# Optimization experiments

Measured on AMD Instinct MI355X. Metric: run time of the kernel, lower is better.

Reference implementation:

```python
import jax, jax.numpy as jnp
import numpy as np

NEG_INF = -10000.0
ALPHA = 0.2      # LeakyReLU slope
EPS = 1e-5       # LayerNorm eps
B, N, D = 8, 2048, 128


def setup_inputs() -> dict:
    key = jax.random.key(0)
    ks = jax.random.split(key, 8)
    x = jax.random.normal(ks[0], (B, N, D), dtype=jnp.float32)
    adj_bool = jax.random.randint(ks[1], (B, N, N), 0, 2, dtype=jnp.int32)
    node_mask = jax.random.randint(ks[2], (B, N), 0, 2, dtype=jnp.int32)
    s = 1.0 / np.sqrt(D)
    W = jax.random.uniform(ks[3], (D, D), jnp.float32, -s, s)    # fc weight (in->out)
    a_l = jax.random.uniform(ks[4], (D,), jnp.float32, -s, s)    # attn_l weight
    a_r = jax.random.uniform(ks[5], (D,), jnp.float32, -s, s)    # attn_r weight
    gamma = jnp.ones((D,), jnp.float32)                          # LayerNorm weight
    beta = jnp.zeros((D,), jnp.float32)                          # LayerNorm bias
    return {"x": x, "adj_bool": adj_bool, "node_mask": node_mask,
            "W": W, "a_l": a_l, "a_r": a_r, "gamma": gamma, "beta": beta}


def reference(x, adj_bool, node_mask, W, a_l, a_r, gamma, beta):
    m = node_mask.astype(x.dtype)[..., None]           # [B,N,1]
    x = x * m
    h = jnp.einsum('bnd,de->bne', x, W)                # [B,N,D]
    e_l = jnp.einsum('bnd,d->bn', h, a_l)              # [B,N]
    e_r = jnp.einsum('bnd,d->bn', h, a_r)              # [B,N]
    e = e_l[:, :, None] + e_r[:, None, :]              # [B,N,N]
    e = jnp.where(e > 0, e, ALPHA * e)                 # LeakyReLU
    pair = (node_mask[:, :, None] * node_mask[:, None, :]) > 0
    allowed = (adj_bool > 0) & pair
    e = jnp.where(allowed, e, NEG_INF)
    attn = jax.nn.softmax(e, axis=-1)                  # finite (NEG_INF fill), nan_to_num is a no-op
    out = jnp.einsum('bij,bjd->bid', attn, h)          # dropout in eval mode = identity
    out = (out + x) * m                                # residual (ind==outd), then node mask
    mu = jnp.mean(out, axis=-1, keepdims=True)
    var = jnp.var(out, axis=-1, keepdims=True)
    out = (out - mu) * jax.lax.rsqrt(var + EPS) * gamma + beta
    return out
```

## Files before the change

### kernel.cpp

```cpp
#include <hip/hip_runtime.h>
#include <stdint.h>


#define BB 8
#define NN 2048
#define DD 128
#define LN_EPS 1e-5f

#define FC_BLOCKS 512
#define PK_BLOCKS 4096

typedef __attribute__((ext_vector_type(8))) short short8;
typedef __attribute__((ext_vector_type(4))) float f32x4;

__device__ __forceinline__ unsigned pk_bf16(float a, float b) {
    unsigned ua = __float_as_uint(a); ua += 0x7FFFu + ((ua >> 16) & 1u);
    unsigned ub = __float_as_uint(b); ub += 0x7FFFu + ((ub >> 16) & 1u);
    return (ua >> 16) | (ub & 0xFFFF0000u);
}

__global__ __launch_bounds__(256) void prep_kernel(
    const float* __restrict__ x, const int* __restrict__ mask,
    const float* __restrict__ W, const float* __restrict__ a_l,
    const float* __restrict__ a_r, const int* __restrict__ adj,
    unsigned short* __restrict__ hTX, float* __restrict__ el,
    float* __restrict__ er, unsigned* __restrict__ adjw)
{
    __shared__ __align__(16) unsigned char smem[41984];

    const int t   = threadIdx.x;
    const int blk = blockIdx.x;

    if (blk >= FC_BLOCKS) {
        const int w  = t >> 6, ln = t & 63;
        const int r  = (blk - FC_BLOCKS) * 4 + w;
        const int b  = r >> 11;
        const int4* arow4 = (const int4*)(adj + (size_t)r * NN);
        const int4* mrow4 = (const int4*)(mask + ((size_t)b << 11));

        unsigned myword = 0;
#pragma unroll
        for (int c = 0; c < 8; ++c) {
            int4 a = arow4[c * 64 + ln];
            int4 m = mrow4[c * 64 + ln];
            unsigned nib = (unsigned)(a.x & m.x & 1)
                         | ((unsigned)(a.y & m.y & 1) << 1)
                         | ((unsigned)(a.z & m.z & 1) << 2)
                         | ((unsigned)(a.w & m.w & 1) << 3);
            unsigned v = nib << ((ln & 7) * 4);
            v |= __shfl_xor(v, 1, 64);
            v |= __shfl_xor(v, 2, 64);
            v |= __shfl_xor(v, 4, 64);
            unsigned got = __shfl(v, (ln & 7) * 8, 64);
            if ((ln >> 3) == c) myword = got;
        }
        adjw[(size_t)r * 64 + ln] = myword;
        return;
    }

    const int b   = blk >> 6;
    const int it  = blk & 63;
    const int i0  = it * 32;
    const int half = it & 1;
    const int jt   = it >> 1;

    unsigned short* WT2 = (unsigned short*)smem;
    unsigned* WT2u = (unsigned*)smem;
    unsigned* xs2u = (unsigned*)(smem + 32768);
    unsigned* hws  = (unsigned*)(smem + 32768);

#pragma unroll 4
    for (int s = 0; s < 32; ++s) {
        int g  = t + 256 * s;
        int e  = g & 127;
        int kp = g >> 7;
        float w0 = W[(size_t)(2 * kp) * DD + e];
        float w1 = W[(size_t)(2 * kp + 1) * DD + e];
        WT2u[((kp >> 2) * 128 + e) * 4 + (kp & 3)] = pk_bf16(w0, w1);
    }

    {
#pragma unroll
        for (int s4 = 0; s4 < 4; ++s4) {
            int idx = t + 256 * s4;
            int i = idx >> 5, c4 = idx & 31;
            float4 f = *(const float4*)(x + ((size_t)(b * NN + i0 + i)) * DD
                                          + c4 * 4);
            float mm = (float)mask[b * NN + i0 + i];
            unsigned p0 = pk_bf16(f.x * mm, f.y * mm);
            unsigned p1 = pk_bf16(f.z * mm, f.w * mm);
            unsigned* dst = xs2u + ((size_t)((c4 >> 1) * 32 + i)) * 4
                          + (c4 & 1) * 2;
            dst[0] = p0; dst[1] = p1;
        }
    }
    __syncthreads();

    const int lane = t & 63, w = t >> 6;
    const int row = lane & 15, grp = lane >> 4;

    f32x4 acc[2][2];
#pragma unroll
    for (int mt = 0; mt < 2; ++mt)
#pragma unroll
        for (int nt = 0; nt < 2; ++nt) acc[mt][nt] = (f32x4)0.f;

#pragma unroll
    for (int kk = 0; kk < 4; ++kk) {
        const unsigned short* cb = WT2 + ((size_t)(kk * 4 + grp) * 128) * 8;
        short8 A0 = *(const short8*)(cb + (w * 32 + row) * 8);
        short8 A1 = *(const short8*)(cb + (w * 32 + 16 + row) * 8);
        const unsigned short* xb = (const unsigned short*)xs2u
                                 + ((size_t)(kk * 4 + grp) * 32) * 8;
#pragma unroll
        for (int nt = 0; nt < 2; ++nt) {
            short8 Bv = *(const short8*)(xb + (nt * 16 + row) * 8);
            acc[0][nt] = __builtin_amdgcn_mfma_f32_16x16x32_bf16(A0, Bv, acc[0][nt], 0, 0, 0);
            acc[1][nt] = __builtin_amdgcn_mfma_f32_16x16x32_bf16(A1, Bv, acc[1][nt], 0, 0, 0);
        }
    }
    __syncthreads();

    float al8[2][4], ar8[2][4];
#pragma unroll
    for (int mt = 0; mt < 2; ++mt)
#pragma unroll
        for (int reg = 0; reg < 4; ++reg) {
            int e = w * 32 + mt * 16 + grp * 4 + reg;
            al8[mt][reg] = a_l[e];
            ar8[mt][reg] = a_r[e];
        }
    float* sE = (float*)smem;
#pragma unroll
    for (int nt = 0; nt < 2; ++nt) {
        float pl = 0.f, pr = 0.f;
#pragma unroll
        for (int mt = 0; mt < 2; ++mt)
#pragma unroll
            for (int reg = 0; reg < 4; ++reg) {
                pl += acc[mt][nt][reg] * al8[mt][reg];
                pr += acc[mt][nt][reg] * ar8[mt][reg];
            }
        pl += __shfl_xor(pl, 16, 64); pl += __shfl_xor(pl, 32, 64);
        pr += __shfl_xor(pr, 16, 64); pr += __shfl_xor(pr, 32, 64);
        if (grp == 0) {
            sE[w * 32 + nt * 16 + row]       = pl;
            sE[128 + w * 32 + nt * 16 + row] = pr;
        }
    }

    unsigned* hw = hws + w * 576;
#pragma unroll
    for (int mt = 0; mt < 2; ++mt)
#pragma unroll
        for (int nt = 0; nt < 2; ++nt)
#pragma unroll
            for (int reg = 0; reg < 4; ++reg) {
                float v  = acc[mt][nt][reg];
                float vp = __shfl_xor(v, 1, 64);
                if ((row & 1) == 0)
                    hw[(mt * 16 + grp * 4 + reg) * 18 + ((nt * 16 + row) >> 1)] =
                        pk_bf16(v, vp);
            }
    {
        const int dl = lane & 31, part = lane >> 5;
        unsigned short* dstb = hTX + (size_t)b * (DD * NN) + (size_t)jt * 8192;
#pragma unroll
        for (int pp = 0; pp < 2; ++pp) {
            int ic2 = part * 2 + pp;
            uint4 q = *(const uint4*)(hw + dl * 18 + ic2 * 4);
            *(uint4*)(dstb + ((size_t)((half * 4 + ic2) * 128 + w * 32 + dl)) * 8) = q;
        }
    }

    __syncthreads();
    if (t < 32)
        el[b * NN + i0 + t] = sE[t] + sE[32 + t] + sE[64 + t] + sE[96 + t];
    else if (t < 64) {
        int i = t - 32;
        er[b * NN + i0 + i] = sE[128 + i] + sE[160 + i] + sE[192 + i] + sE[224 + i];
    }
}

__global__ __launch_bounds__(256, 4) void attn_kernel(
    const float* __restrict__ x, const unsigned* __restrict__ adjw,
    const int* __restrict__ mask, const unsigned short* __restrict__ hTX,
    const float* __restrict__ el, const float* __restrict__ er,
    const float* __restrict__ gamma, const float* __restrict__ beta,
    float* __restrict__ outp)
{
    __shared__ __align__(16) float sAcc[4][16][132];
    __shared__ float sL[4][16];

    const int t    = threadIdx.x;
    const int w    = t >> 6;
    const int lane = t & 63;
    const int row  = lane & 15;
    const int grp  = lane >> 4;
    const int b    = blockIdx.x >> 7;
    const int it   = blockIdx.x & 127;
    const int i0   = it * 16;
    const int gi   = i0 + row;

    const float el_r = el[b * NN + gi];
    const int   mi   = mask[b * NN + gi];
    const unsigned* aw_row = adjw + ((size_t)(b * NN + gi)) * 64;
    const float* er_b = er + b * NN;
    const unsigned short* hTX_b = hTX + (size_t)b * DD * NN;

    f32x4 acc[8];
#pragma unroll
    for (int nb = 0; nb < 8; ++nb) acc[nb] = (f32x4)0.f;
    float l_lane = 0.f;

    const int jt0  = w * 8;
    const int voff = (grp * 128 + row) * 8;

    union BU { int4 q; short8 v; };
    union AU { unsigned u[4]; short8 v; };

#pragma unroll 1
    for (int jj = 0; jj < 8; ++jj) {
        const int jt = jt0 + jj;
        const uint2 wv = *(const uint2*)(aw_row + jt * 2);
        const unsigned w0 = mi ? wv.x : 0u;
        const unsigned w1 = mi ? wv.y : 0u;
        const int jb = jt * 64 + grp * 8;
        const unsigned short* hp = hTX_b + (size_t)jt * 8192 + voff;

        {
            BU bf[8];
#pragma unroll
            for (int nb = 0; nb < 8; ++nb)
                bf[nb].q = *(const int4*)(hp + nb * 128);
            const float4 e0 = *(const float4*)(er_b + jb);
            const float4 e1 = *(const float4*)(er_b + jb + 4);
            const float ev[8] = {e0.x,e0.y,e0.z,e0.w, e1.x,e1.y,e1.z,e1.w};
            float p[8];
#pragma unroll
            for (int u = 0; u < 8; ++u) {
                float s = el_r + ev[u];
                s = fmaxf(s, 0.2f * s);
                p[u] = ((w0 >> (grp * 8 + u)) & 1u) ? __expf(s) : 0.f;
                l_lane += p[u];
            }
            AU A;
#pragma unroll
            for (int k = 0; k < 4; ++k) A.u[k] = pk_bf16(p[2*k], p[2*k+1]);
#pragma unroll
            for (int nb = 0; nb < 8; ++nb)
                acc[nb] = __builtin_amdgcn_mfma_f32_16x16x32_bf16(A.v, bf[nb].v, acc[nb], 0, 0, 0);
        }
        {
            BU bf[8];
#pragma unroll
            for (int nb = 0; nb < 8; ++nb)
                bf[nb].q = *(const int4*)(hp + 4096 + nb * 128);
            const float4 e2 = *(const float4*)(er_b + jb + 32);
            const float4 e3 = *(const float4*)(er_b + jb + 36);
            const float ev[8] = {e2.x,e2.y,e2.z,e2.w, e3.x,e3.y,e3.z,e3.w};
            float p[8];
#pragma unroll
            for (int u = 0; u < 8; ++u) {
                float s = el_r + ev[u];
                s = fmaxf(s, 0.2f * s);
                p[u] = ((w1 >> (grp * 8 + u)) & 1u) ? __expf(s) : 0.f;
                l_lane += p[u];
            }
            AU A;
#pragma unroll
            for (int k = 0; k < 4; ++k) A.u[k] = pk_bf16(p[2*k], p[2*k+1]);
#pragma unroll
            for (int nb = 0; nb < 8; ++nb)
                acc[nb] = __builtin_amdgcn_mfma_f32_16x16x32_bf16(A.v, bf[nb].v, acc[nb], 0, 0, 0);
        }
    }

    l_lane += __shfl_xor(l_lane, 16, 64);
    l_lane += __shfl_xor(l_lane, 32, 64);
    if (grp == 0) sL[w][row] = l_lane;
#pragma unroll
    for (int nb = 0; nb < 8; ++nb)
#pragma unroll
        for (int reg = 0; reg < 4; ++reg)
            sAcc[w][grp * 4 + reg][nb * 16 + row] = acc[nb][reg];
    __syncthreads();

    const int crow = t >> 4;
    const int cl   = t & 15;
    const int gr   = i0 + crow;

    const float Ls   = sL[0][crow] + sL[1][crow] + sL[2][crow] + sL[3][crow];
    const float linv = Ls > 0.f ? 1.0f / Ls : 0.f;
    const float mrow = (float)mask[b * NN + gr];
    const float* xrow = x + ((size_t)(b * NN + gr)) * DD;

    float vbuf[8];
    float s1 = 0.f, s2 = 0.f;
#pragma unroll
    for (int h = 0; h < 2; ++h) {
        const int c0 = cl * 8 + h * 4;
        float4 xv = *(const float4*)(xrow + c0);
        float4 a0 = *(const float4*)(&sAcc[0][crow][c0]);
        float4 a1 = *(const float4*)(&sAcc[1][crow][c0]);
        float4 a2 = *(const float4*)(&sAcc[2][crow][c0]);
        float4 a3 = *(const float4*)(&sAcc[3][crow][c0]);
        float tv;
        tv = ((a0.x + a1.x + a2.x + a3.x) * linv + xv.x) * mrow;
        vbuf[h*4+0] = tv; s1 += tv; s2 += tv*tv;
        tv = ((a0.y + a1.y + a2.y + a3.y) * linv + xv.y) * mrow;
        vbuf[h*4+1] = tv; s1 += tv; s2 += tv*tv;
        tv = ((a0.z + a1.z + a2.z + a3.z) * linv + xv.z) * mrow;
        vbuf[h*4+2] = tv; s1 += tv; s2 += tv*tv;
        tv = ((a0.w + a1.w + a2.w + a3.w) * linv + xv.w) * mrow;
        vbuf[h*4+3] = tv; s1 += tv; s2 += tv*tv;
    }
#pragma unroll
    for (int off = 1; off < 16; off <<= 1) {
        s1 += __shfl_xor(s1, off, 64);
        s2 += __shfl_xor(s2, off, 64);
    }
    const float mu  = s1 * (1.0f / DD);
    const float var = s2 * (1.0f / DD) - mu * mu;
    const float rsd = rsqrtf(var + LN_EPS);

    float* orow = outp + ((size_t)(b * NN + gr)) * DD;
#pragma unroll
    for (int h = 0; h < 2; ++h) {
        const int c0 = cl * 8 + h * 4;
        float4 g  = *(const float4*)(gamma + c0);
        float4 be = *(const float4*)(beta + c0);
        float4 o;
        o.x = (vbuf[h*4+0] - mu) * rsd * g.x + be.x;
        o.y = (vbuf[h*4+1] - mu) * rsd * g.y + be.y;
        o.z = (vbuf[h*4+2] - mu) * rsd * g.z + be.z;
        o.w = (vbuf[h*4+3] - mu) * rsd * g.w + be.w;
        *(float4*)(orow + c0) = o;
    }
}

extern "C" void kernel_launch(void* const* d_in, const int* in_sizes, int n_in,
                              void* d_out, int out_size, void* d_ws, size_t ws_size,
                              hipStream_t stream) {
    const float* x     = (const float*)d_in[0];
    const int*   adj   = (const int*)d_in[1];
    const int*   maskp = (const int*)d_in[2];
    const float* W     = (const float*)d_in[3];
    const float* a_l   = (const float*)d_in[4];
    const float* a_r   = (const float*)d_in[5];
    const float* gamma = (const float*)d_in[6];
    const float* beta  = (const float*)d_in[7];
    float*       outp  = (float*)d_out;

    unsigned short* hTX = (unsigned short*)d_ws;
    float* el = (float*)(hTX + (size_t)BB * DD * NN);
    float* er = el + (size_t)BB * NN;
    unsigned* adjw = (unsigned*)(er + (size_t)BB * NN);

    prep_kernel<<<FC_BLOCKS + PK_BLOCKS, 256, 0, stream>>>(
        x, maskp, W, a_l, a_r, adj, hTX, el, er, adjw);
    attn_kernel<<<BB * (NN / 16), 256, 0, stream>>>(x, adjw, maskp, hTX,
                                                    el, er, gamma, beta, outp);
}
```

Before: 236.8 us.

## Software-pipeline hTX/er/adj loads in attention loop and shrink prep LDS

The attention loop now double-buffers the bf16 B-fragment loads: the second half-tile is loaded at the start of each iteration and the next tile's first half, adjacency word and er values are prefetched between the two MFMA groups. This is meant to hide global-memory latency behind the MFMA and exp work. The extra live registers force launch bounds down from 4 to 3 waves/blocks per SIMD. Separately, the prep kernel's hws scratch buffer is moved to overlap the W buffer region, reducing LDS from 41984 to 40960 bytes, which assumes W is no longer needed when hws is written.

```diff
diff --git a/kernel.cpp b/kernel.cpp
--- a/kernel.cpp
+++ b/kernel.cpp
@@ -26,7 +26,7 @@
     unsigned short* __restrict__ hTX, float* __restrict__ el,
     float* __restrict__ er, unsigned* __restrict__ adjw)
 {
-    __shared__ __align__(16) unsigned char smem[41984];
+    __shared__ __align__(16) unsigned char smem[40960];
 
     const int t   = threadIdx.x;
     const int blk = blockIdx.x;
@@ -67,7 +67,7 @@
     unsigned short* WT2 = (unsigned short*)smem;
     unsigned* WT2u = (unsigned*)smem;
     unsigned* xs2u = (unsigned*)(smem + 32768);
-    unsigned* hws  = (unsigned*)(smem + 32768);
+    unsigned* hws  = (unsigned*)(smem + 1024);
 
 #pragma unroll 4
     for (int s = 0; s < 32; ++s) {
@@ -182,7 +182,7 @@
     }
 }
 
-__global__ __launch_bounds__(256, 4) void attn_kernel(
+__global__ __launch_bounds__(256, 3) void attn_kernel(
     const float* __restrict__ x, const unsigned* __restrict__ adjw,
     const int* __restrict__ mask, const unsigned short* __restrict__ hTX,
     const float* __restrict__ el, const float* __restrict__ er,
@@ -219,22 +219,37 @@
     union BU { int4 q; short8 v; };
     union AU { unsigned u[4]; short8 v; };
 
+    BU bfA[8];
+    uint2 wv;
+    float4 e0, e1;
+    {
+        const unsigned short* hp = hTX_b + (size_t)jt0 * 8192 + voff;
+#pragma unroll
+        for (int nb = 0; nb < 8; ++nb)
+            bfA[nb].q = *(const int4*)(hp + nb * 128);
+        wv = *(const uint2*)(aw_row + jt0 * 2);
+        const int jb = jt0 * 64 + grp * 8;
+        e0 = *(const float4*)(er_b + jb);
+        e1 = *(const float4*)(er_b + jb + 4);
+    }
+
 #pragma unroll 1
     for (int jj = 0; jj < 8; ++jj) {
         const int jt = jt0 + jj;
-        const uint2 wv = *(const uint2*)(aw_row + jt * 2);
+        const int jb = jt * 64 + grp * 8;
+        const unsigned short* hp = hTX_b + (size_t)jt * 8192 + voff;
+
+        BU bfB[8];
+#pragma unroll
+        for (int nb = 0; nb < 8; ++nb)
+            bfB[nb].q = *(const int4*)(hp + 4096 + nb * 128);
+        const float4 e2 = *(const float4*)(er_b + jb + 32);
+        const float4 e3 = *(const float4*)(er_b + jb + 36);
+
         const unsigned w0 = mi ? wv.x : 0u;
         const unsigned w1 = mi ? wv.y : 0u;
-        const int jb = jt * 64 + grp * 8;
-        const unsigned short* hp = hTX_b + (size_t)jt * 8192 + voff;
 
         {
-            BU bf[8];
-#pragma unroll
-            for (int nb = 0; nb < 8; ++nb)
-                bf[nb].q = *(const int4*)(hp + nb * 128);
-            const float4 e0 = *(const float4*)(er_b + jb);
-            const float4 e1 = *(const float4*)(er_b + jb + 4);
             const float ev[8] = {e0.x,e0.y,e0.z,e0.w, e1.x,e1.y,e1.z,e1.w};
             float p[8];
 #pragma unroll
@@ -249,15 +264,22 @@
             for (int k = 0; k < 4; ++k) A.u[k] = pk_bf16(p[2*k], p[2*k+1]);
 #pragma unroll
             for (int nb = 0; nb < 8; ++nb)
-                acc[nb] = __builtin_amdgcn_mfma_f32_16x16x32_bf16(A.v, bf[nb].v, acc[nb], 0, 0, 0);
-        }
+                acc[nb] = __builtin_amdgcn_mfma_f32_16x16x32_bf16(A.v, bfA[nb].v, acc[nb], 0, 0, 0);
+        }
+
         {
-            BU bf[8];
+            const int jtn = jj < 7 ? jt + 1 : jt;
+            const unsigned short* hpn = hTX_b + (size_t)jtn * 8192 + voff;
 #pragma unroll
             for (int nb = 0; nb < 8; ++nb)
-                bf[nb].q = *(const int4*)(hp + 4096 + nb * 128);
-            const float4 e2 = *(const float4*)(er_b + jb + 32);
-            const float4 e3 = *(const float4*)(er_b + jb + 36);
+                bfA[nb].q = *(const int4*)(hpn + nb * 128);
+            wv = *(const uint2*)(aw_row + jtn * 2);
+            const int jbn = jtn * 64 + grp * 8;
+            e0 = *(const float4*)(er_b + jbn);
+            e1 = *(const float4*)(er_b + jbn + 4);
+        }
+
+        {
             const float ev[8] = {e2.x,e2.y,e2.z,e2.w, e3.x,e3.y,e3.z,e3.w};
             float p[8];
 #pragma unroll
@@ -272,7 +294,7 @@
             for (int k = 0; k < 4; ++k) A.u[k] = pk_bf16(p[2*k], p[2*k+1]);
 #pragma unroll
             for (int nb = 0; nb < 8; ++nb)
-                acc[nb] = __builtin_amdgcn_mfma_f32_16x16x32_bf16(A.v, bf[nb].v, acc[nb], 0, 0, 0);
+                acc[nb] = __builtin_amdgcn_mfma_f32_16x16x32_bf16(A.v, bfB[nb].v, acc[nb], 0, 0, 0);
         }
     }
 
```

Result: no change. 236.3 us (-0.2%).
